# Kernel tuning notes

Hardware: AMD Instinct MI355X
Metric: run time of the kernel (lower is better)

Reference implementation:

```python
import jax, jax.numpy as jnp
import numpy as np

B, N, DIM, H, DH = 2, 1024, 1024, 8, 64
DI = H * DH  # 512
K = 4        # depthwise conv kernel
EPS = 1.1920929e-07  # float32 eps (torch RMSNorm default)


def setup_inputs() -> dict:
    key = jax.random.key(0)
    ks = jax.random.split(key, 12)
    s = lambda k, shape, sc=0.02: jax.random.normal(k, shape, jnp.float32) * sc
    return dict(
        x=jax.random.normal(ks[0], (B, N, DIM), jnp.float32),
        w_rms=jnp.ones((DIM,), jnp.float32),
        wq=s(ks[1], (DIM, DI)), wk=s(ks[2], (DIM, DI)), wv=s(ks[3], (DIM, DI)),
        wo=s(ks[4], (DI, DIM)),
        conv_q=s(ks[5], (DIM, K), 0.3), conv_k=s(ks[6], (DIM, K), 0.3), conv_v=s(ks[7], (DIM, K), 0.3),
        gamma_q=jnp.ones((H, 1, DH), jnp.float32), gamma_k=jnp.ones((H, 1, DH), jnp.float32),
        lr_w=s(ks[8], (DIM, H)), lr_b=jnp.full((H,), -4.0, jnp.float32),
        decay_w=s(ks[9], (DIM, H)), decay_b=jnp.full((H,), 4.0, jnp.float32),
        mom_w=s(ks[10], (DIM, H)), mom_b=jnp.full((H,), 2.0, jnp.float32),
    )


def rmsnorm(x, w):
    return x * jax.lax.rsqrt(jnp.mean(x * x, -1, keepdims=True) + EPS) * w


def mh_rmsnorm(x, gamma):  # x: (b, h, n, d)
    rms = jnp.sqrt(jnp.sum(x * x, -1, keepdims=True)) * (DH ** -0.5)
    return x / jnp.maximum(rms, 1e-8) * gamma


def dwconv(x, w):  # x: (b, n, dim), w: (dim, K) depthwise, padding K//2 -> length n+1
    y = jax.lax.conv_general_dilated(
        x.transpose(0, 2, 1), w[:, None, :], (1,), [(K // 2, K // 2)],
        feature_group_count=DIM, dimension_numbers=('NCW', 'OIW', 'NCW'))
    return y.transpose(0, 2, 1)


def gated_scan(a, x):  # h_t = a_t h_{t-1} + x_t, h_{-1}=0; a:(bh,t), x:(bh,t,d,d)
    def combine(c1, c2):
        a1, x1 = c1
        a2, x2 = c2
        return a1 * a2, a2 * x1 + x2
    _, h = jax.lax.associative_scan(combine, (a[..., None, None], x), axis=1)
    return h


def reference(x, w_rms, wq, wk, wv, wo, conv_q, conv_k, conv_v,
              gamma_q, gamma_k, lr_w, lr_b, decay_w, decay_b, mom_w, mom_b):
    b, n, _ = x.shape
    xa = rmsnorm(x, w_rms)
    qi, ki, vi = dwconv(xa, conv_q), dwconv(xa, conv_k), dwconv(xa, conv_v)
    split = lambda t: t.reshape(b, -1, H, DH).transpose(0, 2, 1, 3)[:, :, :n]  # (b,h,n,d)
    q = mh_rmsnorm(split(qi @ wq), gamma_q)
    k = mh_rmsnorm(split(ki @ wk), gamma_k)
    v = split(vi @ wv)
    fq = q.reshape(b * H, n, DH)
    fk = k.reshape(b * H, n, DH)
    fv = v.reshape(b * H, n, DH)
    sig = jax.nn.sigmoid
    lr = sig(xa @ lr_w + lr_b).transpose(0, 2, 1).reshape(b * H, n)
    decay = sig(xa @ decay_w + decay_b).transpose(0, 2, 1).reshape(b * H, n)
    mom = sig(xa @ mom_w + mom_b).transpose(0, 2, 1).reshape(b * H, n)
    # S_ref = S0 = 0 (fresh state) => pred = 0, delta_vec = -v
    g = jnp.einsum('bti,btj->btij', -fv, fk)          # (bh, n, d, d)
    Z = gated_scan(mom, g)                             # momentum scan
    S = gated_scan(decay, -lr[..., None, None] * Z)    # memory scan
    S_prev = jnp.concatenate([jnp.zeros_like(S[:, :1]), S[:, :-1]], axis=1)
    y = jnp.einsum('btdp,btp->btd', S_prev, fq)        # retrieval y_t = S_{t-1} psi_t
    y = y.reshape(b, H, n, DH).transpose(0, 2, 1, 3).reshape(b, n, DI)
    return y @ wo
```

## Files before the change

kernel.cpp:

```cpp
#include <hip/hip_runtime.h>
#include <math.h>

#define DEV __device__ __forceinline__

constexpr int Bb   = 2;
constexpr int Seq  = 1024;
constexpr int Dim  = 1024;
constexpr int Hh   = 8;
constexpr int Dh   = 64;
constexpr int Di   = 512;
constexpr int BN   = Bb * Seq;
constexpr int NSEQ = Bb * Hh;
constexpr int CHUNK = 32;
constexpr int CLEN  = Seq / CHUNK;
constexpr float EPSV = 1.1920929e-07f;
constexpr int NT2  = 8;
constexpr int KSPL = 8;

typedef _Float16 half8 __attribute__((ext_vector_type(8)));
typedef float    f32x4 __attribute__((ext_vector_type(4)));

DEV float bf2f(unsigned short u) {
  union { unsigned int i; float f; } x; x.i = ((unsigned int)u) << 16; return x.f;
}
DEV unsigned short f2bf(float f) {
  union { float f; unsigned int i; } x; x.f = f;
  unsigned int r = x.i + 0x7fffu + ((x.i >> 16) & 1u);
  return (unsigned short)(r >> 16);
}
DEV float ldin(const void* p, int f32, size_t i) {
  if (f32) return ((const float*)p)[i];
  return bf2f(((const unsigned short*)p)[i]);
}
DEV void ld4(const void* p, int f32, size_t i, float* dst) {
  if (f32) {
    float4 u = *(const float4*)((const float*)p + i);
    dst[0] = u.x; dst[1] = u.y; dst[2] = u.z; dst[3] = u.w;
  } else {
    ushort4 u = *(const ushort4*)((const unsigned short*)p + i);
    dst[0] = bf2f(u.x); dst[1] = bf2f(u.y); dst[2] = bf2f(u.z); dst[3] = bf2f(u.w);
  }
}
DEV int sniff_vote(const void* p, int n, int tid) {
  int j = 2 * tid, valid = 0, bad = 0;
  if (j < n) {
    valid = 1;
    float v = bf2f(((const unsigned short*)p)[j]);
    float a = fabsf(v);
    if (!(a >= 1e-12f && a <= 1e4f)) bad = 1;
  }
#pragma unroll
  for (int m = 1; m < 64; m <<= 1) { valid += __shfl_xor(valid, m); bad += __shfl_xor(bad, m); }
  return (2 * bad > valid) ? 1 : 0;
}

struct InPtrs { const void* p[17]; int n[17]; };

__global__ __launch_bounds__(256) void k_prep_all(
    InPtrs ip,
    int* __restrict__ flags,
    _Float16* __restrict__ wqT, _Float16* __restrict__ wkT,
    _Float16* __restrict__ wvT, _Float16* __restrict__ woT,
    _Float16* __restrict__ WgT,
    _Float16* __restrict__ wcq, _Float16* __restrict__ wck,
    _Float16* __restrict__ wcv,
    float* __restrict__ gqf, float* __restrict__ gkf, float* __restrict__ gbf)
{
  int blk = blockIdx.x;
  int tid = threadIdx.x;
  __shared__ int sfl[8];

  if (blk < 1024) {
    int z = blk >> 8, bx = blk & 15, by = (blk >> 4) & 15;
    int idx = (z == 0) ? 2 : ((z == 1) ? 3 : ((z == 2) ? 4 : 5));
    const void* src = ip.p[idx];
    _Float16* dst   = (z == 0) ? wqT : ((z == 1) ? wkT : ((z == 2) ? wvT : woT));
    int Kd = (z < 3) ? Dim : Di;
    int Nn = (z < 3) ? Di : Dim;
    int n0 = bx * 64, k0 = by * 64;
    if (n0 >= Nn || k0 >= Kd) return;

    if (tid < 64) { int f = sniff_vote(src, ip.n[idx], tid); if (tid == 0) sfl[0] = f; }
    __syncthreads();
    int f = sfl[0];

    __shared__ float tile[64][65];
    int r = tid >> 4, c4 = (tid & 15) * 4;
#pragma unroll
    for (int rr = 0; rr < 4; ++rr) {
      int k = rr * 16 + r;
      ld4(src, f, (size_t)(k0 + k) * Nn + n0 + c4, &tile[k][c4]);
    }
    __syncthreads();
#pragma unroll
    for (int rr = 0; rr < 4; ++rr) {
      int n = rr * 16 + r;
      _Float16 o4[4];
#pragma unroll
      for (int j = 0; j < 4; ++j) o4[j] = (_Float16)tile[c4 + j][n];
      *(ushort4*)&dst[(size_t)(n0 + n) * Kd + k0 + c4] = *(ushort4*)o4;
    }
  } else if (blk < 1088) {
    int row = blk - 1024;
    if (row < 24) {
      int g = row >> 3, h = row & 7;
      int idx = (g == 0) ? 11 : ((g == 1) ? 13 : 15);
      const void* W = ip.p[idx];
      if (tid < 64) { int f = sniff_vote(W, ip.n[idx], tid); if (tid == 0) sfl[0] = f; }
      __syncthreads();
      int f = sfl[0];
#pragma unroll
      for (int it = 0; it < 4; ++it) {
        int d = it * 256 + tid;
        WgT[(size_t)row * Dim + d] = (_Float16)ldin(W, f, (size_t)d * Hh + h);
      }
    } else {
#pragma unroll
      for (int it = 0; it < 4; ++it)
        WgT[(size_t)row * Dim + it * 256 + tid] = (_Float16)0.f;
    }
  } else if (blk < 1104) {
    if (tid < 64) {
      int f6 = sniff_vote(ip.p[6], ip.n[6], tid);
      int f7 = sniff_vote(ip.p[7], ip.n[7], tid);
      int f8 = sniff_vote(ip.p[8], ip.n[8], tid);
      if (tid == 0) { sfl[0] = f6; sfl[1] = f7; sfl[2] = f8; }
    }
    __syncthreads();
    int e = (blk - 1088) * 256 + tid;
    wcq[e] = (_Float16)ldin(ip.p[6], sfl[0], e);
    wck[e] = (_Float16)ldin(ip.p[7], sfl[1], e);
    wcv[e] = (_Float16)ldin(ip.p[8], sfl[2], e);
  } else {
    __shared__ int allf[17];
    for (int ii = 0; ii < 17; ++ii) {
      if (tid < 64) {
        int f = sniff_vote(ip.p[ii], ip.n[ii], tid);
        if (tid == 0) { flags[ii] = f; allf[ii] = f; }
      }
    }
    __syncthreads();
    int f9 = allf[9], f10 = allf[10];
    for (int i = tid; i < Di; i += 256) {
      gqf[i] = ldin(ip.p[9], f9, i);
      gkf[i] = ldin(ip.p[10], f10, i);
    }
    if (tid < 24) {
      int g = tid >> 3, h = tid & 7;
      int idx = (g == 0) ? 12 : ((g == 1) ? 14 : 16);
      gbf[tid] = ldin(ip.p[idx], allf[idx], h);
    }
  }
}

__global__ __launch_bounds__(256) void k_rmsconv(
    const void* __restrict__ x, const void* __restrict__ w_rms,
    const int* __restrict__ flags,
    const _Float16* __restrict__ wcq, const _Float16* __restrict__ wck,
    const _Float16* __restrict__ wcv,
    _Float16* __restrict__ xaf,
    _Float16* __restrict__ qc, _Float16* __restrict__ kc,
    _Float16* __restrict__ vc)
{
  constexpr int NR = NT2 + 3;
  __shared__ _Float16 xas[NR][Dim];
  int tb = blockIdx.x, b = blockIdx.y;
  int t0 = tb * NT2;
  int tid = threadIdx.x, lane = tid & 63, wv = tid >> 6;
  int fx = flags[0], fw = flags[1];
  int e0 = lane * 16;

  float wr[16];
#pragma unroll
  for (int q = 0; q < 4; ++q) ld4(w_rms, fw, e0 + q * 4, &wr[q * 4]);

  for (int rr = wv; rr < NR; rr += 4) {
    int r = t0 - 2 + rr;
    float xv[16];
    bool inr = (r >= 0 && r < Seq);
    if (inr) {
      size_t rb = (size_t)(b * Seq + r) * Dim + e0;
#pragma unroll
      for (int q = 0; q < 4; ++q) ld4(x, fx, rb + q * 4, &xv[q * 4]);
    } else {
#pragma unroll
      for (int j = 0; j < 16; ++j) xv[j] = 0.f;
    }
    float ss = 0.f;
#pragma unroll
    for (int j = 0; j < 16; ++j) ss = fmaf(xv[j], xv[j], ss);
#pragma unroll
    for (int m = 1; m < 64; m <<= 1) ss += __shfl_xor(ss, m);
    float scale = rsqrtf(ss * (1.0f / Dim) + EPSV);

    _Float16 o[16];
#pragma unroll
    for (int j = 0; j < 16; ++j) o[j] = (_Float16)(xv[j] * scale * wr[j]);
    *(uint4*)&xas[rr][e0]     = *(uint4*)&o[0];
    *(uint4*)&xas[rr][e0 + 8] = *(uint4*)&o[8];
    if (inr && r >= t0 && r < t0 + NT2) {
      size_t ob = (size_t)(b * Seq + r) * Dim + e0;
      *(uint4*)&xaf[ob]     = *(uint4*)&o[0];
      *(uint4*)&xaf[ob + 8] = *(uint4*)&o[8];
    }
  }
  __syncthreads();

  int c0 = tid * 4;
  _Float16 lwq[16], lwk[16], lwv[16];
  *(uint4*)&lwq[0] = *(const uint4*)&wcq[c0 * 4];
  *(uint4*)&lwq[8] = *(const uint4*)&wcq[c0 * 4 + 8];
  *(uint4*)&lwk[0] = *(const uint4*)&wck[c0 * 4];
  *(uint4*)&lwk[8] = *(const uint4*)&wck[c0 * 4 + 8];
  *(uint4*)&lwv[0] = *(const uint4*)&wcv[c0 * 4];
  *(uint4*)&lwv[8] = *(const uint4*)&wcv[c0 * 4 + 8];

#pragma unroll
  for (int tt = 0; tt < NT2; ++tt) {
    float rv[4][4];
#pragma unroll
    for (int k = 0; k < 4; ++k) {
      _Float16 hx[4];
      *(ushort4*)hx = *(const ushort4*)&xas[tt + k][c0];
#pragma unroll
      for (int j = 0; j < 4; ++j) rv[k][j] = (float)hx[j];
    }
    _Float16 tq[4], tk[4], tv[4];
#pragma unroll
    for (int j = 0; j < 4; ++j) {
      float aq = rv[0][j] * (float)lwq[j * 4 + 0] + rv[1][j] * (float)lwq[j * 4 + 1]
               + rv[2][j] * (float)lwq[j * 4 + 2] + rv[3][j] * (float)lwq[j * 4 + 3];
      float ak = rv[0][j] * (float)lwk[j * 4 + 0] + rv[1][j] * (float)lwk[j * 4 + 1]
               + rv[2][j] * (float)lwk[j * 4 + 2] + rv[3][j] * (float)lwk[j * 4 + 3];
      float av = rv[0][j] * (float)lwv[j * 4 + 0] + rv[1][j] * (float)lwv[j * 4 + 1]
               + rv[2][j] * (float)lwv[j * 4 + 2] + rv[3][j] * (float)lwv[j * 4 + 3];
      tq[j] = (_Float16)aq; tk[j] = (_Float16)ak; tv[j] = (_Float16)av;
    }
    size_t o = ((size_t)(b * Seq + t0 + tt)) * Dim + c0;
    *(ushort4*)&qc[o] = *(ushort4*)tq;
    *(ushort4*)&kc[o] = *(ushort4*)tk;
    *(ushort4*)&vc[o] = *(ushort4*)tv;
  }
}

__global__ __launch_bounds__(256) void k_mid(
    const _Float16* __restrict__ qc, const _Float16* __restrict__ kc,
    const _Float16* __restrict__ vc,
    const _Float16* __restrict__ wqT, const _Float16* __restrict__ wkT,
    const _Float16* __restrict__ wvT,
    const _Float16* __restrict__ xaf, const _Float16* __restrict__ WgT,
    _Float16* __restrict__ qpre, _Float16* __restrict__ kpre,
    _Float16* __restrict__ vpre,
    float* __restrict__ gpart)
{
  __shared__ __align__(16) _Float16 As[128][40];
  __shared__ __align__(16) _Float16 Bs[64][40];

  int blk = blockIdx.x;
  int tid = threadIdx.x, lane = tid & 63, wv = tid >> 6;
  int mrow = lane & 15, quad = lane >> 4;

  if (blk < 384) {
    int z = blk / 128, rem = blk - z * 128;
    int by = rem >> 3, bx = rem & 7;
    const _Float16* A  = (z == 0) ? qc : ((z == 1) ? kc : vc);
    const _Float16* Bt = (z == 0) ? wqT : ((z == 1) ? wkT : wvT);
    _Float16* C        = (z == 0) ? qpre : ((z == 1) ? kpre : vpre);
    int n0 = bx * 64, m0 = by * 128;
    int wm = wv * 32;
    int ar0 = tid >> 2, ac0 = (tid & 3) * 8;
    int ar1 = (tid + 256) >> 2;

    f32x4 acc[2][4];
#pragma unroll
    for (int mi = 0; mi < 2; ++mi)
#pragma unroll
      for (int ni = 0; ni < 4; ++ni) acc[mi][ni] = (f32x4){0.f, 0.f, 0.f, 0.f};

    for (int kt = 0; kt < Dim; kt += 32) {
      __syncthreads();
      *(uint4*)&As[ar0][ac0] = *(const uint4*)&A[(size_t)(m0 + ar0) * Dim + kt + ac0];
      *(uint4*)&As[ar1][ac0] = *(const uint4*)&A[(size_t)(m0 + ar1) * Dim + kt + ac0];
      *(uint4*)&Bs[ar0][ac0] = *(const uint4*)&Bt[(size_t)(n0 + ar0) * Dim + kt + ac0];
      __syncthreads();

      half8 bfr[4];
#pragma unroll
      for (int ni = 0; ni < 4; ++ni)
        bfr[ni] = *(const half8*)&Bs[ni * 16 + mrow][quad * 8];
#pragma unroll
      for (int mi = 0; mi < 2; ++mi) {
        half8 afr = *(const half8*)&As[wm + mi * 16 + mrow][quad * 8];
#pragma unroll
        for (int ni = 0; ni < 4; ++ni)
          acc[mi][ni] = __builtin_amdgcn_mfma_f32_16x16x32_f16(afr, bfr[ni], acc[mi][ni], 0, 0, 0);
      }
    }

#pragma unroll
    for (int mi = 0; mi < 2; ++mi) {
#pragma unroll
      for (int ni = 0; ni < 4; ++ni) {
        int col = n0 + ni * 16 + mrow;
#pragma unroll
        for (int r2 = 0; r2 < 4; ++r2) {
          int row = m0 + wm + mi * 16 + quad * 4 + r2;
          C[(size_t)row * Di + col] = (_Float16)acc[mi][ni][r2];
        }
      }
    }
  } else {
    int g = blk - 384;
    int m0 = (g & 31) * 64, ks = g >> 5;
    int srow = tid >> 2, scol = (tid & 3) * 8;
    int kbase = ks * (Dim / KSPL);

    f32x4 acc[4];
#pragma unroll
    for (int mi = 0; mi < 4; ++mi) acc[mi] = (f32x4){0.f, 0.f, 0.f, 0.f};

    for (int kt = kbase; kt < kbase + Dim / KSPL; kt += 32) {
      __syncthreads();
      *(uint4*)&As[srow][scol] = *(const uint4*)&xaf[(size_t)(m0 + srow) * Dim + kt + scol];
      *(uint4*)&Bs[srow][scol] = *(const uint4*)&WgT[(size_t)srow * Dim + kt + scol];
      __syncthreads();
      half8 bfr = *(const half8*)&Bs[wv * 16 + mrow][quad * 8];
#pragma unroll
      for (int mi = 0; mi < 4; ++mi) {
        half8 afr = *(const half8*)&As[mi * 16 + mrow][quad * 8];
        acc[mi] = __builtin_amdgcn_mfma_f32_16x16x32_f16(afr, bfr, acc[mi], 0, 0, 0);
      }
    }

    int col = wv * 16 + mrow;
    if (col < 24) {
#pragma unroll
      for (int mi = 0; mi < 4; ++mi) {
#pragma unroll
        for (int r2 = 0; r2 < 4; ++r2) {
          int row = m0 + mi * 16 + quad * 4 + r2;
          gpart[((size_t)ks * BN + row) * 32 + col] = acc[mi][r2];
        }
      }
    }
  }
}

__global__ __launch_bounds__(256) void k_gemm_fin(
    const _Float16* __restrict__ A, const _Float16* __restrict__ Bt,
    void* __restrict__ C, const int* __restrict__ flags, int Nn, int Kd)
{
  __shared__ __align__(16) _Float16 As[128][40];
  __shared__ __align__(16) _Float16 Bs[64][40];

  int tid = threadIdx.x, lane = tid & 63, wv = tid >> 6;
  int n0 = blockIdx.x * 64, m0 = blockIdx.y * 128;
  int mrow = lane & 15, quad = lane >> 4;
  int wm = wv * 32;
  int ar0 = tid >> 2, ac0 = (tid & 3) * 8;
  int ar1 = (tid + 256) >> 2;

  f32x4 acc[2][4];
#pragma unroll
  for (int mi = 0; mi < 2; ++mi)
#pragma unroll
    for (int ni = 0; ni < 4; ++ni) acc[mi][ni] = (f32x4){0.f, 0.f, 0.f, 0.f};

  for (int kt = 0; kt < Kd; kt += 32) {
    __syncthreads();
    *(uint4*)&As[ar0][ac0] = *(const uint4*)&A[(size_t)(m0 + ar0) * Kd + kt + ac0];
    *(uint4*)&As[ar1][ac0] = *(const uint4*)&A[(size_t)(m0 + ar1) * Kd + kt + ac0];
    *(uint4*)&Bs[ar0][ac0] = *(const uint4*)&Bt[(size_t)(n0 + ar0) * Kd + kt + ac0];
    __syncthreads();

    half8 bfr[4];
#pragma unroll
    for (int ni = 0; ni < 4; ++ni)
      bfr[ni] = *(const half8*)&Bs[ni * 16 + mrow][quad * 8];
#pragma unroll
    for (int mi = 0; mi < 2; ++mi) {
      half8 afr = *(const half8*)&As[wm + mi * 16 + mrow][quad * 8];
#pragma unroll
      for (int ni = 0; ni < 4; ++ni)
        acc[mi][ni] = __builtin_amdgcn_mfma_f32_16x16x32_f16(afr, bfr[ni], acc[mi][ni], 0, 0, 0);
    }
  }

  int any_bf16 = 0;
#pragma unroll
  for (int i2 = 0; i2 < 17; ++i2) any_bf16 |= (flags[i2] == 0);

#pragma unroll
  for (int mi = 0; mi < 2; ++mi) {
#pragma unroll
    for (int ni = 0; ni < 4; ++ni) {
      int col = n0 + ni * 16 + mrow;
#pragma unroll
      for (int r2 = 0; r2 < 4; ++r2) {
        int row = m0 + wm + mi * 16 + quad * 4 + r2;
        float v = acc[mi][ni][r2];
        size_t idx = (size_t)row * Nn + col;
        if (any_bf16) ((unsigned short*)C)[idx] = f2bf(v);
        else          ((float*)C)[idx] = v;
      }
    }
  }
}

DEV void load_gates(const float* __restrict__ gpart, const float* __restrict__ gbf,
                    int b, int h, int c, int tid,
                    float* gl, float* gd, float* gm)
{
  if (tid < 96) {
    int which = tid >> 5, t2 = tid & 31;
    int col = which * 8 + h;
    int row = b * Seq + c * CLEN + t2;
    float acc = gbf[col];
#pragma unroll
    for (int ks = 0; ks < KSPL; ++ks)
      acc += gpart[((size_t)ks * BN + row) * 32 + col];
    float sg = 1.f / (1.f + expf(-acc));
    if (which == 0) gl[t2] = sg; else if (which == 1) gd[t2] = sg; else gm[t2] = sg;
  }
}

__global__ __launch_bounds__(256) void k_phaseA(
    const _Float16* __restrict__ kpre, const _Float16* __restrict__ vpre,
    const float* __restrict__ gkf,
    const float* __restrict__ gpart, const float* __restrict__ gbf,
    _Float16* __restrict__ ZS_Z, _Float16* __restrict__ ZS_S,
    float* __restrict__ Mc, float* __restrict__ Dc, float* __restrict__ Wc)
{
  int c = blockIdx.x, s = blockIdx.y;
  int b = s >> 3, h = s & 7;
  int tid = threadIdx.x, lane = tid & 63, wv = tid >> 6;
  int i = tid >> 2, j0 = (tid & 3) * 16;
  __shared__ float kn[CLEN][64], vv[CLEN][64];
  __shared__ float gl[CLEN], gd[CLEN], gm[CLEN];

  {
    int t = tid >> 3, col = (tid & 7) * 8;
    size_t g = ((size_t)(b * Seq + c * CLEN + t)) * Di + h * 64 + col;
    half8 kv = *(const half8*)&kpre[g];
    half8 vvv = *(const half8*)&vpre[g];
#pragma unroll
    for (int j = 0; j < 8; ++j) { kn[t][col + j] = (float)kv[j]; vv[t][col + j] = (float)vvv[j]; }
    load_gates(gpart, gbf, b, h, c, tid, gl, gd, gm);
  }
  __syncthreads();
  {
    float gk = gkf[h * 64 + lane];
#pragma unroll
    for (int tt = 0; tt < 8; ++tt) {
      int t = wv * 8 + tt;
      float kvv = kn[t][lane];
      float ss = kvv * kvv;
#pragma unroll
      for (int m = 1; m < 64; m <<= 1) ss += __shfl_xor(ss, m);
      kn[t][lane] = kvv * (1.f / fmaxf(sqrtf(ss) * 0.125f, 1e-8f)) * gk;
    }
  }
  __syncthreads();

  float Zl[16], Sl[16];
#pragma unroll
  for (int jj = 0; jj < 16; ++jj) { Zl[jj] = 0.f; Sl[jj] = 0.f; }
  float Mcum = 1.f, Dcum = 1.f, wacc = 0.f;

  for (int t = 0; t < CLEN; ++t) {
    float l = gl[t], dd = gd[t], mm = gm[t];
    float vi = vv[t][i];
    Mcum *= mm;
#pragma unroll
    for (int jj = 0; jj < 16; ++jj) {
      Zl[jj] = fmaf(mm, Zl[jj], -vi * kn[t][j0 + jj]);
      Sl[jj] = fmaf(dd, Sl[jj], -l * Zl[jj]);
    }
    wacc = fmaf(dd, wacc, -l * Mcum);
    Dcum *= dd;
  }
  size_t base = ((size_t)(s * CHUNK + c)) * 4096 + (size_t)i * 64 + j0;
  half8 zo0, zo1, so0, so1;
#pragma unroll
  for (int jj = 0; jj < 8; ++jj) {
    zo0[jj] = (_Float16)Zl[jj];     zo1[jj] = (_Float16)Zl[jj + 8];
    so0[jj] = (_Float16)Sl[jj];     so1[jj] = (_Float16)Sl[jj + 8];
  }
  *(half8*)&ZS_Z[base] = zo0; *(half8*)&ZS_Z[base + 8] = zo1;
  *(half8*)&ZS_S[base] = so0; *(half8*)&ZS_S[base + 8] = so1;
  if (tid == 0) {
    Mc[s * CHUNK + c] = Mcum; Dc[s * CHUNK + c] = Dcum; Wc[s * CHUNK + c] = wacc;
  }
}

__global__ __launch_bounds__(256) void k_phaseB(
    _Float16* __restrict__ ZS_Z, _Float16* __restrict__ ZS_S,
    const float* __restrict__ Mc, const float* __restrict__ Dc,
    const float* __restrict__ Wc)
{
  int s = blockIdx.x;
  int e = blockIdx.y * 256 + threadIdx.x;
  float Z = 0.f, S = 0.f;
  for (int c = 0; c < CHUNK; ++c) {
    size_t base = ((size_t)(s * CHUNK + c)) * 4096 + e;
    float mc = Mc[s * CHUNK + c], dc = Dc[s * CHUNK + c], wc = Wc[s * CHUNK + c];
    float zl = (float)ZS_Z[base], sl = (float)ZS_S[base];
    ZS_Z[base] = (_Float16)Z; ZS_S[base] = (_Float16)S;
    S = fmaf(dc, S, fmaf(wc, Z, sl));
    Z = fmaf(mc, Z, zl);
  }
}

__global__ __launch_bounds__(256) void k_phaseC(
    const _Float16* __restrict__ qpre, const _Float16* __restrict__ kpre,
    const _Float16* __restrict__ vpre,
    const float* __restrict__ gqf, const float* __restrict__ gkf,
    const float* __restrict__ gpart, const float* __restrict__ gbf,
    const _Float16* __restrict__ ZS_Z, const _Float16* __restrict__ ZS_S,
    _Float16* __restrict__ yb)
{
  int c = blockIdx.x, s = blockIdx.y;
  int b = s >> 3, h = s & 7;
  int tid = threadIdx.x, lane = tid & 63, wv = tid >> 6;
  int i = tid >> 2, j0 = (tid & 3) * 16;
  __shared__ float kn[CLEN][64], vv[CLEN][64], qn[CLEN][64];
  __shared__ float gl[CLEN], gd[CLEN], gm[CLEN];

  float Zi_[16], Si_[16], Zl[16], Sl[16];
  size_t base = ((size_t)(s * CHUNK + c)) * 4096 + (size_t)i * 64 + j0;
  {
    half8 z0 = *(const half8*)&ZS_Z[base], z1 = *(const half8*)&ZS_Z[base + 8];
    half8 s0 = *(const half8*)&ZS_S[base], s1 = *(const half8*)&ZS_S[base + 8];
#pragma unroll
    for (int jj = 0; jj < 8; ++jj) {
      Zi_[jj] = (float)z0[jj]; Zi_[jj + 8] = (float)z1[jj];
      Si_[jj] = (float)s0[jj]; Si_[jj + 8] = (float)s1[jj];
      Zl[jj] = 0.f; Zl[jj + 8] = 0.f; Sl[jj] = 0.f; Sl[jj + 8] = 0.f;
    }
  }
  {
    int t = tid >> 3, col = (tid & 7) * 8;
    size_t g = ((size_t)(b * Seq + c * CLEN + t)) * Di + h * 64 + col;
    half8 kv = *(const half8*)&kpre[g];
    half8 vvv = *(const half8*)&vpre[g];
    half8 qv = *(const half8*)&qpre[g];
#pragma unroll
    for (int j = 0; j < 8; ++j) {
      kn[t][col + j] = (float)kv[j]; vv[t][col + j] = (float)vvv[j];
      qn[t][col + j] = (float)qv[j];
    }
    load_gates(gpart, gbf, b, h, c, tid, gl, gd, gm);
  }
  __syncthreads();
  {
    float gk = gkf[h * 64 + lane];
    float gq = gqf[h * 64 + lane];
#pragma unroll
    for (int tt = 0; tt < 8; ++tt) {
      int t = wv * 8 + tt;
      float kvv = kn[t][lane];
      float ssk = kvv * kvv;
      float qvv = qn[t][lane];
      float ssq = qvv * qvv;
#pragma unroll
      for (int m = 1; m < 64; m <<= 1) { ssk += __shfl_xor(ssk, m); ssq += __shfl_xor(ssq, m); }
      kn[t][lane] = kvv * (1.f / fmaxf(sqrtf(ssk) * 0.125f, 1e-8f)) * gk;
      qn[t][lane] = qvv * (1.f / fmaxf(sqrtf(ssq) * 0.125f, 1e-8f)) * gq;
    }
  }
  __syncthreads();

  float Mcum = 1.f, Dcum = 1.f, wacc = 0.f;
  float Dprev = 1.f, wprev = 0.f;

  for (int t = 0; t < CLEN; ++t) {
    float l = gl[t], dd = gd[t], mm = gm[t];

    float yp = 0.f;
#pragma unroll
    for (int jj = 0; jj < 16; ++jj) {
      float tmp = fmaf(Dprev, Si_[jj], fmaf(wprev, Zi_[jj], Sl[jj]));
      yp = fmaf(tmp, qn[t][j0 + jj], yp);
    }
    yp += __shfl_xor(yp, 1);
    yp += __shfl_xor(yp, 2);
    if ((tid & 3) == 0)
      yb[((size_t)(b * Seq + c * CLEN + t)) * Di + h * 64 + i] = (_Float16)yp;

    float vi = vv[t][i];
    Mcum *= mm;
#pragma unroll
    for (int jj = 0; jj < 16; ++jj) {
      Zl[jj] = fmaf(mm, Zl[jj], -vi * kn[t][j0 + jj]);
      Sl[jj] = fmaf(dd, Sl[jj], -l * Zl[jj]);
    }
    wacc = fmaf(dd, wacc, -l * Mcum);
    Dcum *= dd;
    Dprev = Dcum; wprev = wacc;
  }
}

extern "C" void kernel_launch(void* const* d_in, const int* in_sizes, int n_in,
                              void* d_out, int out_size, void* d_ws, size_t ws_size,
                              hipStream_t stream) {
  InPtrs ip;
  for (int i = 0; i < 17; ++i) { ip.p[i] = d_in[i]; ip.n[i] = in_sizes[i]; }

  char* p = (char*)d_ws;
  auto take = [&](size_t bytes) -> char* {
    char* q = p; p += (bytes + 255) & ~(size_t)255; return q;
  };
  int* flags           = (int*)take(32 * 4);
  _Float16* xaf        = (_Float16*)take((size_t)BN * Dim * 2);
  _Float16* qc         = (_Float16*)take((size_t)BN * Dim * 2);
  _Float16* kc         = (_Float16*)take((size_t)BN * Dim * 2);
  _Float16* vc         = (_Float16*)take((size_t)BN * Dim * 2);
  _Float16* qpre       = (_Float16*)take((size_t)BN * Di * 2);
  _Float16* kpre       = (_Float16*)take((size_t)BN * Di * 2);
  _Float16* vpre       = (_Float16*)take((size_t)BN * Di * 2);
  float* gpart         = (float*)take((size_t)KSPL * BN * 32 * 4);
  float* Mc            = (float*)take((size_t)NSEQ * CHUNK * 4);
  float* Dc            = (float*)take((size_t)NSEQ * CHUNK * 4);
  float* Wc            = (float*)take((size_t)NSEQ * CHUNK * 4);
  _Float16* wqT        = (_Float16*)take((size_t)Di * Dim * 2);
  _Float16* wkT        = (_Float16*)take((size_t)Di * Dim * 2);
  _Float16* wvT        = (_Float16*)take((size_t)Di * Dim * 2);
  _Float16* woT        = (_Float16*)take((size_t)Dim * Di * 2);
  _Float16* WgT        = (_Float16*)take((size_t)64 * Dim * 2);
  _Float16* wcq        = (_Float16*)take((size_t)Dim * 4 * 2);
  _Float16* wck        = (_Float16*)take((size_t)Dim * 4 * 2);
  _Float16* wcv        = (_Float16*)take((size_t)Dim * 4 * 2);
  float* gqf           = (float*)take(Di * 4);
  float* gkf           = (float*)take(Di * 4);
  float* gbf           = (float*)take(32 * 4);
  _Float16* ZS_Z       = qc;
  _Float16* ZS_S       = kc;
  _Float16* yb         = vc;

  k_prep_all<<<1105, 256, 0, stream>>>(ip, flags, wqT, wkT, wvT, woT, WgT,
                                       wcq, wck, wcv, gqf, gkf, gbf);

  k_rmsconv<<<dim3(Seq / NT2, Bb), 256, 0, stream>>>(
      d_in[0], d_in[1], flags, wcq, wck, wcv, xaf, qc, kc, vc);

  k_mid<<<640, 256, 0, stream>>>(qc, kc, vc, wqT, wkT, wvT, xaf, WgT,
                                 qpre, kpre, vpre, gpart);

  k_phaseA<<<dim3(CHUNK, NSEQ), 256, 0, stream>>>(kpre, vpre, gkf,
                                                  gpart, gbf,
                                                  ZS_Z, ZS_S, Mc, Dc, Wc);
  k_phaseB<<<dim3(NSEQ, 16), 256, 0, stream>>>(ZS_Z, ZS_S, Mc, Dc, Wc);
  k_phaseC<<<dim3(CHUNK, NSEQ), 256, 0, stream>>>(qpre, kpre, vpre, gqf, gkf,
                                                  gpart, gbf,
                                                  ZS_Z, ZS_S, yb);

  k_gemm_fin<<<dim3(Dim / 64, BN / 128), 256, 0, stream>>>(
      yb, woT, d_out, flags, Dim, Di);
}
```

Baseline: 186.3 us.

## Fuse rmsnorm/conv into prep kernel and fold inter-chunk scan into phase C

Merges the RMSNorm plus depthwise-conv kernel into the weight-prep launch, so those blocks sniff input dtypes and read conv weights directly, and the separate conv-weight conversion is dropped. It also removes the phase-B inter-chunk scan kernel: each phase-C block now recomputes its chunk-initial Z/S state by scanning all previous chunk summaries itself. This saves two launches and the phase-B read-modify-write pass. The cost is redundant O(chunk) recomputation in phase C, up to 31 extra chunk loads for late chunks, and a larger shared-memory footprint for every prep block.

New measurement: 189.8 us. About the same (+1.9%).

```diff
diff --git a/kernel.cpp b/kernel.cpp
--- a/kernel.cpp
+++ b/kernel.cpp
@@ -41,6 +41,26 @@
     dst[0] = bf2f(u.x); dst[1] = bf2f(u.y); dst[2] = bf2f(u.z); dst[3] = bf2f(u.w);
   }
 }
+DEV void ldc16(const void* p, int f32, size_t base, _Float16* dst) {
+  if (f32) {
+#pragma unroll
+    for (int q = 0; q < 4; ++q) {
+      float4 u = *(const float4*)((const float*)p + base + q * 4);
+      dst[q * 4 + 0] = (_Float16)u.x; dst[q * 4 + 1] = (_Float16)u.y;
+      dst[q * 4 + 2] = (_Float16)u.z; dst[q * 4 + 3] = (_Float16)u.w;
+    }
+  } else {
+#pragma unroll
+    for (int q = 0; q < 2; ++q) {
+      ushort4 u0 = *(const ushort4*)((const unsigned short*)p + base + q * 8);
+      ushort4 u1 = *(const ushort4*)((const unsigned short*)p + base + q * 8 + 4);
+      dst[q * 8 + 0] = (_Float16)bf2f(u0.x); dst[q * 8 + 1] = (_Float16)bf2f(u0.y);
+      dst[q * 8 + 2] = (_Float16)bf2f(u0.z); dst[q * 8 + 3] = (_Float16)bf2f(u0.w);
+      dst[q * 8 + 4] = (_Float16)bf2f(u1.x); dst[q * 8 + 5] = (_Float16)bf2f(u1.y);
+      dst[q * 8 + 6] = (_Float16)bf2f(u1.z); dst[q * 8 + 7] = (_Float16)bf2f(u1.w);
+    }
+  }
+}
 DEV int sniff_vote(const void* p, int n, int tid) {
   int j = 2 * tid, valid = 0, bad = 0;
   if (j < n) {
@@ -56,22 +76,106 @@
 
 struct InPtrs { const void* p[17]; int n[17]; };
 
-__global__ __launch_bounds__(256) void k_prep_all(
+__global__ __launch_bounds__(256) void k_prep_rmsconv(
     InPtrs ip,
     int* __restrict__ flags,
     _Float16* __restrict__ wqT, _Float16* __restrict__ wkT,
     _Float16* __restrict__ wvT, _Float16* __restrict__ woT,
     _Float16* __restrict__ WgT,
-    _Float16* __restrict__ wcq, _Float16* __restrict__ wck,
-    _Float16* __restrict__ wcv,
-    float* __restrict__ gqf, float* __restrict__ gkf, float* __restrict__ gbf)
+    float* __restrict__ gqf, float* __restrict__ gkf, float* __restrict__ gbf,
+    _Float16* __restrict__ xaf,
+    _Float16* __restrict__ qc, _Float16* __restrict__ kc,
+    _Float16* __restrict__ vc)
 {
+  constexpr int NR = NT2 + 3;
+  __shared__ _Float16 xas[NR][Dim];
+  __shared__ float tile[64][65];
+  __shared__ int sfl[8];
+
   int blk = blockIdx.x;
-  int tid = threadIdx.x;
-  __shared__ int sfl[8];
-
-  if (blk < 1024) {
-    int z = blk >> 8, bx = blk & 15, by = (blk >> 4) & 15;
+  int tid = threadIdx.x, lane = tid & 63, wv = tid >> 6;
+
+  if (blk < 256) {
+    int tb = blk >> 1, b = blk & 1;
+    int t0 = tb * NT2;
+    int fx = sniff_vote(ip.p[0], ip.n[0], tid);
+    int fw = sniff_vote(ip.p[1], ip.n[1], tid);
+    int e0 = lane * 16;
+
+    float wr[16];
+#pragma unroll
+    for (int q = 0; q < 4; ++q) ld4(ip.p[1], fw, e0 + q * 4, &wr[q * 4]);
+
+    for (int rr = wv; rr < NR; rr += 4) {
+      int r = t0 - 2 + rr;
+      float xv[16];
+      bool inr = (r >= 0 && r < Seq);
+      if (inr) {
+        size_t rb = (size_t)(b * Seq + r) * Dim + e0;
+#pragma unroll
+        for (int q = 0; q < 4; ++q) ld4(ip.p[0], fx, rb + q * 4, &xv[q * 4]);
+      } else {
+#pragma unroll
+        for (int j = 0; j < 16; ++j) xv[j] = 0.f;
+      }
+      float ss = 0.f;
+#pragma unroll
+      for (int j = 0; j < 16; ++j) ss = fmaf(xv[j], xv[j], ss);
+#pragma unroll
+      for (int m = 1; m < 64; m <<= 1) ss += __shfl_xor(ss, m);
+      float scale = rsqrtf(ss * (1.0f / Dim) + EPSV);
+
+      _Float16 o[16];
+#pragma unroll
+      for (int j = 0; j < 16; ++j) o[j] = (_Float16)(xv[j] * scale * wr[j]);
+      *(uint4*)&xas[rr][e0]     = *(uint4*)&o[0];
+      *(uint4*)&xas[rr][e0 + 8] = *(uint4*)&o[8];
+      if (inr && r >= t0 && r < t0 + NT2) {
+        size_t ob = (size_t)(b * Seq + r) * Dim + e0;
+        *(uint4*)&xaf[ob]     = *(uint4*)&o[0];
+        *(uint4*)&xaf[ob + 8] = *(uint4*)&o[8];
+      }
+    }
+
+    int f6 = sniff_vote(ip.p[6], ip.n[6], tid);
+    int f7 = sniff_vote(ip.p[7], ip.n[7], tid);
+    int f8 = sniff_vote(ip.p[8], ip.n[8], tid);
+    int c0 = tid * 4;
+    _Float16 lwq[16], lwk[16], lwv[16];
+    ldc16(ip.p[6], f6, (size_t)c0 * 4, lwq);
+    ldc16(ip.p[7], f7, (size_t)c0 * 4, lwk);
+    ldc16(ip.p[8], f8, (size_t)c0 * 4, lwv);
+    __syncthreads();
+
+#pragma unroll
+    for (int tt = 0; tt < NT2; ++tt) {
+      float rv[4][4];
+#pragma unroll
+      for (int k = 0; k < 4; ++k) {
+        _Float16 hx[4];
+        *(ushort4*)hx = *(const ushort4*)&xas[tt + k][c0];
+#pragma unroll
+        for (int j = 0; j < 4; ++j) rv[k][j] = (float)hx[j];
+      }
+      _Float16 tq[4], tk[4], tv[4];
+#pragma unroll
+      for (int j = 0; j < 4; ++j) {
+        float aq = rv[0][j] * (float)lwq[j * 4 + 0] + rv[1][j] * (float)lwq[j * 4 + 1]
+                 + rv[2][j] * (float)lwq[j * 4 + 2] + rv[3][j] * (float)lwq[j * 4 + 3];
+        float ak = rv[0][j] * (float)lwk[j * 4 + 0] + rv[1][j] * (float)lwk[j * 4 + 1]
+                 + rv[2][j] * (float)lwk[j * 4 + 2] + rv[3][j] * (float)lwk[j * 4 + 3];
+        float av = rv[0][j] * (float)lwv[j * 4 + 0] + rv[1][j] * (float)lwv[j * 4 + 1]
+                 + rv[2][j] * (float)lwv[j * 4 + 2] + rv[3][j] * (float)lwv[j * 4 + 3];
+        tq[j] = (_Float16)aq; tk[j] = (_Float16)ak; tv[j] = (_Float16)av;
+      }
+      size_t o = ((size_t)(b * Seq + t0 + tt)) * Dim + c0;
+      *(ushort4*)&qc[o] = *(ushort4*)tq;
+      *(ushort4*)&kc[o] = *(ushort4*)tk;
+      *(ushort4*)&vc[o] = *(ushort4*)tv;
+    }
+  } else if (blk < 1280) {
+    int bb = blk - 256;
+    int z = bb >> 8, bx = bb & 15, by = (bb >> 4) & 15;
     int idx = (z == 0) ? 2 : ((z == 1) ? 3 : ((z == 2) ? 4 : 5));
     const void* src = ip.p[idx];
     _Float16* dst   = (z == 0) ? wqT : ((z == 1) ? wkT : ((z == 2) ? wvT : woT));
@@ -84,7 +188,6 @@
     __syncthreads();
     int f = sfl[0];
 
-    __shared__ float tile[64][65];
     int r = tid >> 4, c4 = (tid & 15) * 4;
 #pragma unroll
     for (int rr = 0; rr < 4; ++rr) {
@@ -100,8 +203,8 @@
       for (int j = 0; j < 4; ++j) o4[j] = (_Float16)tile[c4 + j][n];
       *(ushort4*)&dst[(size_t)(n0 + n) * Kd + k0 + c4] = *(ushort4*)o4;
     }
-  } else if (blk < 1088) {
-    int row = blk - 1024;
+  } else if (blk < 1344) {
+    int row = blk - 1280;
     if (row < 24) {
       int g = row >> 3, h = row & 7;
       int idx = (g == 0) ? 11 : ((g == 1) ? 13 : 15);
@@ -119,18 +222,6 @@
       for (int it = 0; it < 4; ++it)
         WgT[(size_t)row * Dim + it * 256 + tid] = (_Float16)0.f;
     }
-  } else if (blk < 1104) {
-    if (tid < 64) {
-      int f6 = sniff_vote(ip.p[6], ip.n[6], tid);
-      int f7 = sniff_vote(ip.p[7], ip.n[7], tid);
-      int f8 = sniff_vote(ip.p[8], ip.n[8], tid);
-      if (tid == 0) { sfl[0] = f6; sfl[1] = f7; sfl[2] = f8; }
-    }
-    __syncthreads();
-    int e = (blk - 1088) * 256 + tid;
-    wcq[e] = (_Float16)ldin(ip.p[6], sfl[0], e);
-    wck[e] = (_Float16)ldin(ip.p[7], sfl[1], e);
-    wcv[e] = (_Float16)ldin(ip.p[8], sfl[2], e);
   } else {
     __shared__ int allf[17];
     for (int ii = 0; ii < 17; ++ii) {
@@ -150,96 +241,6 @@
       int idx = (g == 0) ? 12 : ((g == 1) ? 14 : 16);
       gbf[tid] = ldin(ip.p[idx], allf[idx], h);
     }
-  }
-}
-
-__global__ __launch_bounds__(256) void k_rmsconv(
-    const void* __restrict__ x, const void* __restrict__ w_rms,
-    const int* __restrict__ flags,
-    const _Float16* __restrict__ wcq, const _Float16* __restrict__ wck,
-    const _Float16* __restrict__ wcv,
-    _Float16* __restrict__ xaf,
-    _Float16* __restrict__ qc, _Float16* __restrict__ kc,
-    _Float16* __restrict__ vc)
-{
-  constexpr int NR = NT2 + 3;
-  __shared__ _Float16 xas[NR][Dim];
-  int tb = blockIdx.x, b = blockIdx.y;
-  int t0 = tb * NT2;
-  int tid = threadIdx.x, lane = tid & 63, wv = tid >> 6;
-  int fx = flags[0], fw = flags[1];
-  int e0 = lane * 16;
-
-  float wr[16];
-#pragma unroll
-  for (int q = 0; q < 4; ++q) ld4(w_rms, fw, e0 + q * 4, &wr[q * 4]);
-
-  for (int rr = wv; rr < NR; rr += 4) {
-    int r = t0 - 2 + rr;
-    float xv[16];
-    bool inr = (r >= 0 && r < Seq);
-    if (inr) {
-      size_t rb = (size_t)(b * Seq + r) * Dim + e0;
-#pragma unroll
-      for (int q = 0; q < 4; ++q) ld4(x, fx, rb + q * 4, &xv[q * 4]);
-    } else {
-#pragma unroll
-      for (int j = 0; j < 16; ++j) xv[j] = 0.f;
-    }
-    float ss = 0.f;
-#pragma unroll
-    for (int j = 0; j < 16; ++j) ss = fmaf(xv[j], xv[j], ss);
-#pragma unroll
-    for (int m = 1; m < 64; m <<= 1) ss += __shfl_xor(ss, m);
-    float scale = rsqrtf(ss * (1.0f / Dim) + EPSV);
-
-    _Float16 o[16];
-#pragma unroll
-    for (int j = 0; j < 16; ++j) o[j] = (_Float16)(xv[j] * scale * wr[j]);
-    *(uint4*)&xas[rr][e0]     = *(uint4*)&o[0];
-    *(uint4*)&xas[rr][e0 + 8] = *(uint4*)&o[8];
-    if (inr && r >= t0 && r < t0 + NT2) {
-      size_t ob = (size_t)(b * Seq + r) * Dim + e0;
-      *(uint4*)&xaf[ob]     = *(uint4*)&o[0];
-      *(uint4*)&xaf[ob + 8] = *(uint4*)&o[8];
-    }
-  }
-  __syncthreads();
-
-  int c0 = tid * 4;
-  _Float16 lwq[16], lwk[16], lwv[16];
-  *(uint4*)&lwq[0] = *(const uint4*)&wcq[c0 * 4];
-  *(uint4*)&lwq[8] = *(const uint4*)&wcq[c0 * 4 + 8];
-  *(uint4*)&lwk[0] = *(const uint4*)&wck[c0 * 4];
-  *(uint4*)&lwk[8] = *(const uint4*)&wck[c0 * 4 + 8];
-  *(uint4*)&lwv[0] = *(const uint4*)&wcv[c0 * 4];
-  *(uint4*)&lwv[8] = *(const uint4*)&wcv[c0 * 4 + 8];
-
-#pragma unroll
-  for (int tt = 0; tt < NT2; ++tt) {
-    float rv[4][4];
-#pragma unroll
-    for (int k = 0; k < 4; ++k) {
-      _Float16 hx[4];
-      *(ushort4*)hx = *(const ushort4*)&xas[tt + k][c0];
-#pragma unroll
-      for (int j = 0; j < 4; ++j) rv[k][j] = (float)hx[j];
-    }
-    _Float16 tq[4], tk[4], tv[4];
-#pragma unroll
-    for (int j = 0; j < 4; ++j) {
-      float aq = rv[0][j] * (float)lwq[j * 4 + 0] + rv[1][j] * (float)lwq[j * 4 + 1]
-               + rv[2][j] * (float)lwq[j * 4 + 2] + rv[3][j] * (float)lwq[j * 4 + 3];
-      float ak = rv[0][j] * (float)lwk[j * 4 + 0] + rv[1][j] * (float)lwk[j * 4 + 1]
-               + rv[2][j] * (float)lwk[j * 4 + 2] + rv[3][j] * (float)lwk[j * 4 + 3];
-      float av = rv[0][j] * (float)lwv[j * 4 + 0] + rv[1][j] * (float)lwv[j * 4 + 1]
-               + rv[2][j] * (float)lwv[j * 4 + 2] + rv[3][j] * (float)lwv[j * 4 + 3];
-      tq[j] = (_Float16)aq; tk[j] = (_Float16)ak; tv[j] = (_Float16)av;
-    }
-    size_t o = ((size_t)(b * Seq + t0 + tt)) * Dim + c0;
-    *(ushort4*)&qc[o] = *(ushort4*)tq;
-    *(ushort4*)&kc[o] = *(ushort4*)tk;
-    *(ushort4*)&vc[o] = *(ushort4*)tv;
   }
 }
 
@@ -493,30 +494,14 @@
   }
 }
 
-__global__ __launch_bounds__(256) void k_phaseB(
-    _Float16* __restrict__ ZS_Z, _Float16* __restrict__ ZS_S,
-    const float* __restrict__ Mc, const float* __restrict__ Dc,
-    const float* __restrict__ Wc)
-{
-  int s = blockIdx.x;
-  int e = blockIdx.y * 256 + threadIdx.x;
-  float Z = 0.f, S = 0.f;
-  for (int c = 0; c < CHUNK; ++c) {
-    size_t base = ((size_t)(s * CHUNK + c)) * 4096 + e;
-    float mc = Mc[s * CHUNK + c], dc = Dc[s * CHUNK + c], wc = Wc[s * CHUNK + c];
-    float zl = (float)ZS_Z[base], sl = (float)ZS_S[base];
-    ZS_Z[base] = (_Float16)Z; ZS_S[base] = (_Float16)S;
-    S = fmaf(dc, S, fmaf(wc, Z, sl));
-    Z = fmaf(mc, Z, zl);
-  }
-}
-
 __global__ __launch_bounds__(256) void k_phaseC(
     const _Float16* __restrict__ qpre, const _Float16* __restrict__ kpre,
     const _Float16* __restrict__ vpre,
     const float* __restrict__ gqf, const float* __restrict__ gkf,
     const float* __restrict__ gpart, const float* __restrict__ gbf,
     const _Float16* __restrict__ ZS_Z, const _Float16* __restrict__ ZS_S,
+    const float* __restrict__ Mc, const float* __restrict__ Dc,
+    const float* __restrict__ Wc,
     _Float16* __restrict__ yb)
 {
   int c = blockIdx.x, s = blockIdx.y;
@@ -527,17 +512,24 @@
   __shared__ float gl[CLEN], gd[CLEN], gm[CLEN];
 
   float Zi_[16], Si_[16], Zl[16], Sl[16];
-  size_t base = ((size_t)(s * CHUNK + c)) * 4096 + (size_t)i * 64 + j0;
-  {
-    half8 z0 = *(const half8*)&ZS_Z[base], z1 = *(const half8*)&ZS_Z[base + 8];
-    half8 s0 = *(const half8*)&ZS_S[base], s1 = *(const half8*)&ZS_S[base + 8];
+#pragma unroll
+  for (int jj = 0; jj < 16; ++jj) { Zi_[jj] = 0.f; Si_[jj] = 0.f; Zl[jj] = 0.f; Sl[jj] = 0.f; }
+  for (int cc = 0; cc < c; ++cc) {
+    size_t cb = ((size_t)(s * CHUNK + cc)) * 4096 + (size_t)i * 64 + j0;
+    half8 z0 = *(const half8*)&ZS_Z[cb], z1 = *(const half8*)&ZS_Z[cb + 8];
+    half8 s0 = *(const half8*)&ZS_S[cb], s1 = *(const half8*)&ZS_S[cb + 8];
+    float mc = Mc[s * CHUNK + cc], dc = Dc[s * CHUNK + cc], wc = Wc[s * CHUNK + cc];
 #pragma unroll
     for (int jj = 0; jj < 8; ++jj) {
-      Zi_[jj] = (float)z0[jj]; Zi_[jj + 8] = (float)z1[jj];
-      Si_[jj] = (float)s0[jj]; Si_[jj + 8] = (float)s1[jj];
-      Zl[jj] = 0.f; Zl[jj + 8] = 0.f; Sl[jj] = 0.f; Sl[jj + 8] = 0.f;
-    }
-  }
+      float zl0 = (float)z0[jj], sl0 = (float)s0[jj];
+      float zl1 = (float)z1[jj], sl1 = (float)s1[jj];
+      Si_[jj]     = fmaf(dc, Si_[jj],     fmaf(wc, Zi_[jj],     sl0));
+      Zi_[jj]     = fmaf(mc, Zi_[jj],     zl0);
+      Si_[jj + 8] = fmaf(dc, Si_[jj + 8], fmaf(wc, Zi_[jj + 8], sl1));
+      Zi_[jj + 8] = fmaf(mc, Zi_[jj + 8], zl1);
+    }
+  }
+
   {
     int t = tid >> 3, col = (tid & 7) * 8;
     size_t g = ((size_t)(b * Seq + c * CLEN + t)) * Di + h * 64 + col;
@@ -627,9 +619,6 @@
   _Float16* wvT        = (_Float16*)take((size_t)Di * Dim * 2);
   _Float16* woT        = (_Float16*)take((size_t)Dim * Di * 2);
   _Float16* WgT        = (_Float16*)take((size_t)64 * Dim * 2);
-  _Float16* wcq        = (_Float16*)take((size_t)Dim * 4 * 2);
-  _Float16* wck        = (_Float16*)take((size_t)Dim * 4 * 2);
-  _Float16* wcv        = (_Float16*)take((size_t)Dim * 4 * 2);
   float* gqf           = (float*)take(Di * 4);
   float* gkf           = (float*)take(Di * 4);
   float* gbf           = (float*)take(32 * 4);
@@ -637,11 +626,8 @@
   _Float16* ZS_S       = kc;
   _Float16* yb         = vc;
 
-  k_prep_all<<<1105, 256, 0, stream>>>(ip, flags, wqT, wkT, wvT, woT, WgT,
-                                       wcq, wck, wcv, gqf, gkf, gbf);
-
-  k_rmsconv<<<dim3(Seq / NT2, Bb), 256, 0, stream>>>(
-      d_in[0], d_in[1], flags, wcq, wck, wcv, xaf, qc, kc, vc);
+  k_prep_rmsconv<<<1345, 256, 0, stream>>>(ip, flags, wqT, wkT, wvT, woT, WgT,
+                                           gqf, gkf, gbf, xaf, qc, kc, vc);
 
   k_mid<<<640, 256, 0, stream>>>(qc, kc, vc, wqT, wkT, wvT, xaf, WgT,
                                  qpre, kpre, vpre, gpart);
@@ -649,10 +635,9 @@
   k_phaseA<<<dim3(CHUNK, NSEQ), 256, 0, stream>>>(kpre, vpre, gkf,
                                                   gpart, gbf,
                                                   ZS_Z, ZS_S, Mc, Dc, Wc);
-  k_phaseB<<<dim3(NSEQ, 16), 256, 0, stream>>>(ZS_Z, ZS_S, Mc, Dc, Wc);
   k_phaseC<<<dim3(CHUNK, NSEQ), 256, 0, stream>>>(qpre, kpre, vpre, gqf, gkf,
                                                   gpart, gbf,
-                                                  ZS_Z, ZS_S, yb);
+                                                  ZS_Z, ZS_S, Mc, Dc, Wc, yb);
 
   k_gemm_fin<<<dim3(Dim / 64, BN / 128), 256, 0, stream>>>(
       yb, woT, d_out, flags, Dim, Di);
```
